# Performance work log

Hardware: AMD Instinct MI355X
Metric: run time of the kernel (lower is better)

The kernel has to match this reference:

```python
import jax, jax.numpy as jnp
import numpy as np

D_MODEL = 1024
D_FF = 1024
NUM_EXPERTS = 8
TOP_K = 2


def setup_inputs() -> dict:
    key = jax.random.key(0)
    ks = jax.random.split(key, 5)
    s_in = 1.0 / np.sqrt(D_MODEL)
    s_ff = 1.0 / np.sqrt(D_FF)
    return {
        "x": jax.random.normal(ks[0], (4, 2048, D_MODEL), dtype=jnp.float32),
        "gate_w": jax.random.normal(ks[1], (NUM_EXPERTS, D_MODEL), dtype=jnp.float32) * s_in,
        # torch Linear weight layout: [out_features, in_features], stacked over experts
        "w_gate": jax.random.normal(ks[2], (NUM_EXPERTS, D_FF, D_MODEL), dtype=jnp.float32) * s_in,
        "w_up": jax.random.normal(ks[3], (NUM_EXPERTS, D_FF, D_MODEL), dtype=jnp.float32) * s_in,
        "w_down": jax.random.normal(ks[4], (NUM_EXPERTS, D_MODEL, D_FF), dtype=jnp.float32) * s_ff,
    }


def reference(x, gate_w, w_gate, w_up, w_down):
    B, S, D = x.shape
    T = B * S
    E = gate_w.shape[0]
    xt = x.reshape(T, D)

    # Router
    logits = xt @ gate_w.T                      # [T, E]
    probs = jax.nn.softmax(logits, axis=-1)
    top_v, top_i = jax.lax.top_k(probs, TOP_K)  # [T, K]
    top_v = top_v / jnp.sum(top_v, axis=-1, keepdims=True)

    tokens_per_expert = jnp.sum(jax.nn.one_hot(top_i, E, dtype=jnp.float32), axis=(0, 1))  # [E]
    f = tokens_per_expert / jnp.sum(tokens_per_expert)
    P = jnp.mean(probs, axis=0)
    aux_loss = E * jnp.sum(f * P)

    # Combine weights: per-token weight for each expert (sum over top-k slots)
    combine = jnp.zeros((T, E), dtype=x.dtype).at[jnp.arange(T)[:, None], top_i].add(top_v)  # [T, E]

    # Dense per-expert SwiGLU (equivalent math to masked gather/scatter loop)
    g = jnp.einsum('td,efd->etf', xt, w_gate)   # [E, T, F]
    u = jnp.einsum('td,efd->etf', xt, w_up)     # [E, T, F]
    act = jax.nn.silu(g) * u
    eo = jnp.einsum('etf,edf->etd', act, w_down)  # [E, T, D]

    out = jnp.einsum('te,etd->td', combine, eo).reshape(B, S, D)
    return out, aux_loss, tokens_per_expert
```

## Files before the change

### kernel.cpp

```cpp
#include <hip/hip_runtime.h>


#define T_TOK   8192
#define DM      1024
#define DFF     1024
#define NE      8
#define TOTS    (2 * T_TOK)
#define R1_BLK  2048
#define CVT_BLK 2048

typedef __attribute__((ext_vector_type(8))) short bf16x8;
typedef __attribute__((ext_vector_type(4))) float f32x4;

#define ASYNC16(gp, lp) __builtin_amdgcn_global_load_lds( \
    (const __attribute__((address_space(1))) unsigned int*)(gp), \
    (__attribute__((address_space(3))) unsigned int*)(lp), 16, 0, 0)

__device__ __forceinline__ unsigned short f2bf(float f) {
    union { float f; unsigned u; } c; c.f = f;
    unsigned r = c.u + 0x7fffu + ((c.u >> 16) & 1u);
    return (unsigned short)(r >> 16);
}
__device__ __forceinline__ float bf2f(unsigned short h) {
    union { unsigned u; float f; } c; c.u = ((unsigned)h) << 16;
    return c.f;
}

__global__ __launch_bounds__(256) void pre_kernel(
    const float* __restrict__ x, const float* __restrict__ gate_w,
    const float* __restrict__ s0, const float* __restrict__ s1, const float* __restrict__ s2,
    unsigned short* __restrict__ d0, unsigned short* __restrict__ d1, unsigned short* __restrict__ d2,
    unsigned short* __restrict__ xb,
    int* __restrict__ topi, float2* __restrict__ topw, float* __restrict__ psum_part)
{
    int tid = threadIdx.x;
    int sub = blockIdx.x >> 1;

    if (blockIdx.x & 1) {
        int base = sub * 256 + tid;
        #pragma unroll
        for (int it = 0; it < 12; ++it) {
            int idx = base + it * (CVT_BLK * 256);
            int seg = idx >> 21;
            int off = (idx & ((1 << 21) - 1)) * 4;
            const float* s = (seg == 0) ? s0 : (seg == 1) ? s1 : s2;
            unsigned short* d = (seg == 0) ? d0 : (seg == 1) ? d1 : d2;
            float4 v = *(const float4*)(s + off);
            ushort4 o;
            o.x = f2bf(v.x); o.y = f2bf(v.y); o.z = f2bf(v.z); o.w = f2bf(v.w);
            *(ushort4*)(d + off) = o;
        }
        return;
    }

    __shared__ float gw[NE * DM];
    __shared__ float blk_psum[NE];

    for (int i = tid; i < NE * DM; i += 256) gw[i] = gate_w[i];
    if (tid < NE) blk_psum[tid] = 0.f;
    __syncthreads();

    int wv = tid >> 6, lane = tid & 63;
    int t = sub * 4 + wv;

    float acc[NE];
    #pragma unroll
    for (int e = 0; e < NE; ++e) acc[e] = 0.f;
    const float* xr = x + (size_t)t * DM;
    unsigned short* xbr = xb + (size_t)t * DM;
    #pragma unroll 4
    for (int i = 0; i < DM / 64; ++i) {
        float xv = xr[i * 64 + lane];
        xbr[i * 64 + lane] = f2bf(xv);
        #pragma unroll
        for (int e = 0; e < NE; ++e)
            acc[e] += xv * gw[e * DM + i * 64 + lane];
    }
    #pragma unroll
    for (int e = 0; e < NE; ++e) {
        float v = acc[e];
        #pragma unroll
        for (int s = 32; s > 0; s >>= 1) v += __shfl_xor(v, s, 64);
        acc[e] = v;
    }
    if (lane == 0) {
        float mx = acc[0];
        #pragma unroll
        for (int e = 1; e < NE; ++e) mx = fmaxf(mx, acc[e]);
        float p[NE], sum = 0.f;
        #pragma unroll
        for (int e = 0; e < NE; ++e) { p[e] = expf(acc[e] - mx); sum += p[e]; }
        float inv = 1.f / sum;
        #pragma unroll
        for (int e = 0; e < NE; ++e) { p[e] *= inv; atomicAdd(&blk_psum[e], p[e]); }
        int i1 = 0; float v1 = p[0];
        #pragma unroll
        for (int e = 1; e < NE; ++e) if (p[e] > v1) { v1 = p[e]; i1 = e; }
        int i2 = -1; float v2 = -1.f;
        #pragma unroll
        for (int e = 0; e < NE; ++e) { if (e == i1) continue; if (p[e] > v2) { v2 = p[e]; i2 = e; } }
        float winv = 1.f / (v1 + v2);
        topi[t] = i1 | (i2 << 8);
        topw[t] = make_float2(v1 * winv, v2 * winv);
    }
    __syncthreads();
    if (tid < NE) psum_part[sub * NE + tid] = blk_psum[tid];
}

__global__ __launch_bounds__(1024) void scatfin_kernel(
    const int* __restrict__ topi, const float* __restrict__ psum_part,
    int* __restrict__ elist, int2* __restrict__ cidx,
    int* __restrict__ ecnt, int* __restrict__ ebaseg, float* __restrict__ out_tail)
{
    __shared__ int lcnt[NE], run[NE], cb[NE], ebase[NE];
    __shared__ float parts[NE];
    __shared__ float red[1024];
    int tid = threadIdx.x;

    if (tid < NE) run[tid] = 0;
    __syncthreads();
    #pragma unroll
    for (int ch = 0; ch < T_TOK / 1024; ++ch) {
        int tt = ch * 1024 + tid;
        int pk = topi[tt];
        int e1 = pk & 0xff, e2 = (pk >> 8) & 0xff;
        if (tid < NE) lcnt[tid] = 0;
        __syncthreads();
        int p1 = atomicAdd(&lcnt[e1], 1);
        int p2 = atomicAdd(&lcnt[e2], 1);
        __syncthreads();
        if (tid < NE) { cb[tid] = run[tid]; run[tid] += lcnt[tid]; }
        __syncthreads();
        cidx[tt] = make_int2(cb[e1] + p1, cb[e2] + p2);
    }
    __syncthreads();
    if (tid == 0) {
        int s = 0;
        for (int e = 0; e < NE; ++e) { ebase[e] = s; s += run[e]; }
    }
    __syncthreads();
    #pragma unroll
    for (int ch = 0; ch < T_TOK / 1024; ++ch) {
        int tt = ch * 1024 + tid;
        int pk = topi[tt];
        int e1 = pk & 0xff, e2 = (pk >> 8) & 0xff;
        int2 pp = cidx[tt];
        int r1 = ebase[e1] + pp.x, r2 = ebase[e2] + pp.y;
        elist[r1] = tt;
        elist[r2] = tt;
        cidx[tt] = make_int2(r1, r2);
    }
    if (tid < NE) { ecnt[tid] = run[tid]; ebaseg[tid] = ebase[tid]; }

    int e = tid & 7, b0 = tid >> 3;
    float s = 0.f;
    for (int b = b0; b < R1_BLK; b += 128) s += psum_part[b * NE + e];
    red[tid] = s;
    __syncthreads();
    if (tid < NE) {
        float tot = 0.f;
        #pragma unroll
        for (int j = 0; j < 128; ++j) tot += red[tid + NE * j];
        float P = tot / (float)T_TOK;
        float f = (float)run[tid] / (float)(2 * T_TOK);
        parts[tid] = f * P;
        out_tail[1 + tid] = (float)run[tid];
    }
    __syncthreads();
    if (tid == 0) {
        float s2 = 0.f;
        for (int i = 0; i < NE; ++i) s2 += parts[i];
        out_tail[0] = (float)NE * s2;
    }
}

__global__ __launch_bounds__(256) void gemm1_kernel(
    const unsigned short* __restrict__ xb,
    const unsigned short* __restrict__ wgb,
    const unsigned short* __restrict__ wub,
    const int* __restrict__ elist, const int* __restrict__ ecnt,
    const int* __restrict__ ebaseg,
    unsigned short* __restrict__ Hbuf)
{
    int e = blockIdx.z, mt = blockIdx.y, ft = blockIdx.x;
    int ne = ecnt[e];
    if (mt * 128 >= ne) return;
    int base = ebaseg[e];

    __shared__ unsigned short As[128 * 64];
    __shared__ unsigned short Gs[64 * 64];
    __shared__ unsigned short Us[64 * 64];
    __shared__ int tok[128];

    int tid = threadIdx.x;
    if (tid < 128) {
        int slot = base + mt * 128 + tid;
        tok[tid] = elist[min(slot, TOTS - 1)];
    }
    __syncthreads();

    int wave = tid >> 6, lane = tid & 63;
    int quad = lane >> 4, col = lane & 15;
    int cr = tid >> 3;
    int cl = ((tid & 7) ^ (cr & 7)) * 8;

    const size_t woff = (size_t)e * (size_t)DFF * DM;
    const unsigned short* ap[4];
    #pragma unroll
    for (int j = 0; j < 4; ++j) ap[j] = xb + (size_t)tok[j * 32 + cr] * DM + cl;
    const unsigned short* gp[2];
    const unsigned short* up[2];
    #pragma unroll
    for (int j = 0; j < 2; ++j) {
        gp[j] = wgb + woff + (size_t)(ft * 64 + j * 32 + cr) * DM + cl;
        up[j] = wub + woff + (size_t)(ft * 64 + j * 32 + cr) * DM + cl;
    }
    unsigned short* lA = As + wave * 512;
    unsigned short* lG = Gs + wave * 512;
    unsigned short* lU = Us + wave * 512;

    f32x4 accG[2][4], accU[2][4];
    #pragma unroll
    for (int i = 0; i < 2; ++i)
        #pragma unroll
        for (int n = 0; n < 4; ++n) { accG[i][n] = (f32x4){0,0,0,0}; accU[i][n] = (f32x4){0,0,0,0}; }

    for (int k0 = 0; k0 < DM; k0 += 64) {
        __syncthreads();
        #pragma unroll
        for (int j = 0; j < 4; ++j) ASYNC16(ap[j] + k0, lA + j * 2048);
        #pragma unroll
        for (int j = 0; j < 2; ++j) {
            ASYNC16(gp[j] + k0, lG + j * 2048);
            ASYNC16(up[j] + k0, lU + j * 2048);
        }
        __syncthreads();
        #pragma unroll
        for (int ksoff = 0; ksoff < 8; ksoff += 4) {
            bf16x8 a[2], g[4], u[4];
            #pragma unroll
            for (int i = 0; i < 2; ++i) {
                int m = wave * 32 + i * 16 + col;
                a[i] = *(const bf16x8*)&As[m * 64 + ((quad + ksoff) ^ (m & 7)) * 8];
            }
            #pragma unroll
            for (int n = 0; n < 4; ++n) {
                int nb = n * 16 + col;
                int off = nb * 64 + ((quad + ksoff) ^ (nb & 7)) * 8;
                g[n] = *(const bf16x8*)&Gs[off];
                u[n] = *(const bf16x8*)&Us[off];
            }
            #pragma unroll
            for (int i = 0; i < 2; ++i)
                #pragma unroll
                for (int n = 0; n < 4; ++n) {
                    accG[i][n] = __builtin_amdgcn_mfma_f32_16x16x32_bf16(a[i], g[n], accG[i][n], 0, 0, 0);
                    accU[i][n] = __builtin_amdgcn_mfma_f32_16x16x32_bf16(a[i], u[n], accU[i][n], 0, 0, 0);
                }
        }
    }
    #pragma unroll
    for (int i = 0; i < 2; ++i) {
        #pragma unroll
        for (int r = 0; r < 4; ++r) {
            int pos = mt * 128 + wave * 32 + i * 16 + quad * 4 + r;
            if (pos >= ne) continue;
            unsigned short* hr = Hbuf + (size_t)(base + pos) * DFF + ft * 64 + col;
            #pragma unroll
            for (int n = 0; n < 4; ++n) {
                float gg = accG[i][n][r], uu = accU[i][n][r];
                float h = (gg / (1.f + expf(-gg))) * uu;
                hr[n * 16] = f2bf(h);
            }
        }
    }
}

__global__ __launch_bounds__(256) void gemm2_kernel(
    const unsigned short* __restrict__ Hbuf,
    const unsigned short* __restrict__ wdb,
    const int* __restrict__ ecnt, const int* __restrict__ ebaseg,
    unsigned short* __restrict__ eo)
{
    int e = blockIdx.z, mt = blockIdx.y, dt = blockIdx.x;
    int ne = ecnt[e];
    if (mt * 128 >= ne) return;
    int base = ebaseg[e];

    __shared__ unsigned short As[128 * 64];
    __shared__ unsigned short Bs[128 * 64];

    int tid = threadIdx.x;
    int wave = tid >> 6, lane = tid & 63;
    int quad = lane >> 4, col = lane & 15;
    int wr = (wave >> 1) * 64, wc = (wave & 1) * 64;
    int cr = tid >> 3;
    int cl = ((tid & 7) ^ (cr & 7)) * 8;

    const size_t woff = (size_t)e * (size_t)DM * DFF;
    const unsigned short* ap[4];
    const unsigned short* bp[4];
    #pragma unroll
    for (int j = 0; j < 4; ++j) {
        int hrow = min(base + mt * 128 + j * 32 + cr, TOTS - 1);
        ap[j] = Hbuf + (size_t)hrow * DFF + cl;
        bp[j] = wdb + woff + (size_t)(dt * 128 + j * 32 + cr) * DFF + cl;
    }
    unsigned short* lA = As + wave * 512;
    unsigned short* lB = Bs + wave * 512;

    f32x4 acc[4][4];
    #pragma unroll
    for (int i = 0; i < 4; ++i)
        #pragma unroll
        for (int n = 0; n < 4; ++n) acc[i][n] = (f32x4){0,0,0,0};

    for (int k0 = 0; k0 < DFF; k0 += 64) {
        __syncthreads();
        #pragma unroll
        for (int j = 0; j < 4; ++j) {
            ASYNC16(ap[j] + k0, lA + j * 2048);
            ASYNC16(bp[j] + k0, lB + j * 2048);
        }
        __syncthreads();
        #pragma unroll
        for (int ksoff = 0; ksoff < 8; ksoff += 4) {
            bf16x8 a[4], b[4];
            #pragma unroll
            for (int i = 0; i < 4; ++i) {
                int m = wr + i * 16 + col;
                a[i] = *(const bf16x8*)&As[m * 64 + ((quad + ksoff) ^ (m & 7)) * 8];
            }
            #pragma unroll
            for (int n = 0; n < 4; ++n) {
                int nb = wc + n * 16 + col;
                b[n] = *(const bf16x8*)&Bs[nb * 64 + ((quad + ksoff) ^ (nb & 7)) * 8];
            }
            #pragma unroll
            for (int i = 0; i < 4; ++i)
                #pragma unroll
                for (int n = 0; n < 4; ++n)
                    acc[i][n] = __builtin_amdgcn_mfma_f32_16x16x32_bf16(a[i], b[n], acc[i][n], 0, 0, 0);
        }
    }
    #pragma unroll
    for (int i = 0; i < 4; ++i) {
        #pragma unroll
        for (int r = 0; r < 4; ++r) {
            int pos = mt * 128 + wr + i * 16 + quad * 4 + r;
            if (pos >= ne) continue;
            unsigned short* er = eo + (size_t)(base + pos) * DM + dt * 128 + wc + col;
            #pragma unroll
            for (int n = 0; n < 4; ++n)
                er[n * 16] = f2bf(acc[i][n][r]);
        }
    }
}

__global__ __launch_bounds__(256) void combine_kernel(
    const unsigned short* __restrict__ eo, const float2* __restrict__ topw,
    const int2* __restrict__ cidx, float* __restrict__ out)
{
    int idx = blockIdx.x * 256 + threadIdx.x;
    int t = idx >> 7;
    int c = (idx & 127) << 3;
    float2 w = topw[t];
    int2 rr = cidx[t];
    const unsigned short* p0 = eo + (size_t)rr.x * DM + c;
    const unsigned short* p1 = eo + (size_t)rr.y * DM + c;
    ushort4 a0 = *(const ushort4*)p0;
    ushort4 a1 = *(const ushort4*)(p0 + 4);
    ushort4 b0 = *(const ushort4*)p1;
    ushort4 b1 = *(const ushort4*)(p1 + 4);
    float* orow = out + (size_t)t * DM + c;
    float4 o0, o1;
    o0.x = w.x * bf2f(a0.x) + w.y * bf2f(b0.x);
    o0.y = w.x * bf2f(a0.y) + w.y * bf2f(b0.y);
    o0.z = w.x * bf2f(a0.z) + w.y * bf2f(b0.z);
    o0.w = w.x * bf2f(a0.w) + w.y * bf2f(b0.w);
    o1.x = w.x * bf2f(a1.x) + w.y * bf2f(b1.x);
    o1.y = w.x * bf2f(a1.y) + w.y * bf2f(b1.y);
    o1.z = w.x * bf2f(a1.z) + w.y * bf2f(b1.z);
    o1.w = w.x * bf2f(a1.w) + w.y * bf2f(b1.w);
    *(float4*)orow = o0;
    *(float4*)(orow + 4) = o1;
}

extern "C" void kernel_launch(void* const* d_in, const int* in_sizes, int n_in,
                              void* d_out, int out_size, void* d_ws, size_t ws_size,
                              hipStream_t stream) {
    const float* x      = (const float*)d_in[0];
    const float* gate_w = (const float*)d_in[1];
    const float* w_gate = (const float*)d_in[2];
    const float* w_up   = (const float*)d_in[3];
    const float* w_down = (const float*)d_in[4];
    float* out = (float*)d_out;

    char* p = (char*)d_ws;
    unsigned short* xb   = (unsigned short*)p; p += (size_t)T_TOK * DM * 2;
    unsigned short* wgb  = (unsigned short*)p; p += (size_t)NE * DFF * DM * 2;
    unsigned short* wub  = (unsigned short*)p; p += (size_t)NE * DFF * DM * 2;
    unsigned short* wdb  = (unsigned short*)p; p += (size_t)NE * DM * DFF * 2;
    unsigned short* Hbuf = (unsigned short*)p; p += (size_t)TOTS * DFF * 2;
    int*   elist = (int*)p;   p += (size_t)TOTS * 4;
    int*   ecnt  = (int*)p;   p += NE * 4;
    int*   ebaseg= (int*)p;   p += NE * 4;
    int*   topi  = (int*)p;   p += (size_t)T_TOK * 4;
    float2* topw = (float2*)p; p += (size_t)T_TOK * 8;
    int2*  cidx  = (int2*)p;  p += (size_t)T_TOK * 8;
    float* psum_part = (float*)p; p += (size_t)R1_BLK * NE * 4;
    unsigned short* eo = wgb;

    pre_kernel<<<R1_BLK + CVT_BLK, 256, 0, stream>>>(
        x, gate_w, w_gate, w_up, w_down, wgb, wub, wdb,
        xb, topi, topw, psum_part);
    scatfin_kernel<<<1, 1024, 0, stream>>>(topi, psum_part, elist, cidx, ecnt, ebaseg,
                                           out + (size_t)T_TOK * DM);
    gemm1_kernel<<<dim3(DFF / 64, TOTS / 128, NE), 256, 0, stream>>>(
        xb, wgb, wub, elist, ecnt, ebaseg, Hbuf);
    gemm2_kernel<<<dim3(DM / 128, TOTS / 128, NE), 256, 0, stream>>>(
        Hbuf, wdb, ecnt, ebaseg, eo);
    combine_kernel<<<T_TOK * DM / 8 / 256, 256, 0, stream>>>(eo, topw, cidx, out);
}
```

Baseline: 340.0 us.

## Double-buffer LDS tiles in both expert GEMM kernels to overlap loads with MFMA

Both grouped GEMM kernels now keep two LDS buffers per operand and use a ping-pong main loop. The async global-to-LDS copy of the next K-slice is issued before the MFMA work on the current slice, so load latency can hide behind compute instead of stalling at each barrier. In exchange, LDS use per block doubles (to 64KB in gemm2), which may lower the number of resident blocks per CU. The loop is hardcoded to 16 K-steps of 64.

```diff
diff --git a/kernel.cpp b/kernel.cpp
--- a/kernel.cpp
+++ b/kernel.cpp
@@ -174,6 +174,42 @@
     }
 }
 
+#define G1_STAGE(BUF, KS) do { \
+    _Pragma("unroll") \
+    for (int j = 0; j < 4; ++j) ASYNC16(ap[j] + (KS), &As[BUF][wave * 512] + j * 2048); \
+    _Pragma("unroll") \
+    for (int j = 0; j < 2; ++j) { \
+        ASYNC16(gp[j] + (KS), &Gs[BUF][wave * 512] + j * 2048); \
+        ASYNC16(up[j] + (KS), &Us[BUF][wave * 512] + j * 2048); \
+    } \
+} while (0)
+
+#define G1_COMP(BUF) do { \
+    _Pragma("unroll") \
+    for (int ksoff = 0; ksoff < 8; ksoff += 4) { \
+        bf16x8 a[2], g[4], u[4]; \
+        _Pragma("unroll") \
+        for (int i = 0; i < 2; ++i) { \
+            int m = wave * 32 + i * 16 + col; \
+            a[i] = *(const bf16x8*)&As[BUF][m * 64 + ((quad + ksoff) ^ (m & 7)) * 8]; \
+        } \
+        _Pragma("unroll") \
+        for (int n = 0; n < 4; ++n) { \
+            int nb = n * 16 + col; \
+            int off = nb * 64 + ((quad + ksoff) ^ (nb & 7)) * 8; \
+            g[n] = *(const bf16x8*)&Gs[BUF][off]; \
+            u[n] = *(const bf16x8*)&Us[BUF][off]; \
+        } \
+        _Pragma("unroll") \
+        for (int i = 0; i < 2; ++i) \
+            _Pragma("unroll") \
+            for (int n = 0; n < 4; ++n) { \
+                accG[i][n] = __builtin_amdgcn_mfma_f32_16x16x32_bf16(a[i], g[n], accG[i][n], 0, 0, 0); \
+                accU[i][n] = __builtin_amdgcn_mfma_f32_16x16x32_bf16(a[i], u[n], accU[i][n], 0, 0, 0); \
+            } \
+    } \
+} while (0)
+
 __global__ __launch_bounds__(256) void gemm1_kernel(
     const unsigned short* __restrict__ xb,
     const unsigned short* __restrict__ wgb,
@@ -187,9 +223,9 @@
     if (mt * 128 >= ne) return;
     int base = ebaseg[e];
 
-    __shared__ unsigned short As[128 * 64];
-    __shared__ unsigned short Gs[64 * 64];
-    __shared__ unsigned short Us[64 * 64];
+    __shared__ unsigned short As[2][128 * 64];
+    __shared__ unsigned short Gs[2][64 * 64];
+    __shared__ unsigned short Us[2][64 * 64];
     __shared__ int tok[128];
 
     int tid = threadIdx.x;
@@ -215,9 +251,6 @@
         gp[j] = wgb + woff + (size_t)(ft * 64 + j * 32 + cr) * DM + cl;
         up[j] = wub + woff + (size_t)(ft * 64 + j * 32 + cr) * DM + cl;
     }
-    unsigned short* lA = As + wave * 512;
-    unsigned short* lG = Gs + wave * 512;
-    unsigned short* lU = Us + wave * 512;
 
     f32x4 accG[2][4], accU[2][4];
     #pragma unroll
@@ -225,40 +258,16 @@
         #pragma unroll
         for (int n = 0; n < 4; ++n) { accG[i][n] = (f32x4){0,0,0,0}; accU[i][n] = (f32x4){0,0,0,0}; }
 
-    for (int k0 = 0; k0 < DM; k0 += 64) {
-        __syncthreads();
-        #pragma unroll
-        for (int j = 0; j < 4; ++j) ASYNC16(ap[j] + k0, lA + j * 2048);
-        #pragma unroll
-        for (int j = 0; j < 2; ++j) {
-            ASYNC16(gp[j] + k0, lG + j * 2048);
-            ASYNC16(up[j] + k0, lU + j * 2048);
-        }
-        __syncthreads();
-        #pragma unroll
-        for (int ksoff = 0; ksoff < 8; ksoff += 4) {
-            bf16x8 a[2], g[4], u[4];
-            #pragma unroll
-            for (int i = 0; i < 2; ++i) {
-                int m = wave * 32 + i * 16 + col;
-                a[i] = *(const bf16x8*)&As[m * 64 + ((quad + ksoff) ^ (m & 7)) * 8];
-            }
-            #pragma unroll
-            for (int n = 0; n < 4; ++n) {
-                int nb = n * 16 + col;
-                int off = nb * 64 + ((quad + ksoff) ^ (nb & 7)) * 8;
-                g[n] = *(const bf16x8*)&Gs[off];
-                u[n] = *(const bf16x8*)&Us[off];
-            }
-            #pragma unroll
-            for (int i = 0; i < 2; ++i)
-                #pragma unroll
-                for (int n = 0; n < 4; ++n) {
-                    accG[i][n] = __builtin_amdgcn_mfma_f32_16x16x32_bf16(a[i], g[n], accG[i][n], 0, 0, 0);
-                    accU[i][n] = __builtin_amdgcn_mfma_f32_16x16x32_bf16(a[i], u[n], accU[i][n], 0, 0, 0);
-                }
-        }
-    }
+    G1_STAGE(0, 0);
+    for (int tt = 0; tt < 8; ++tt) {
+        __syncthreads();
+        G1_STAGE(1, (2 * tt + 1) * 64);
+        G1_COMP(0);
+        __syncthreads();
+        if (tt < 7) G1_STAGE(0, (2 * tt + 2) * 64);
+        G1_COMP(1);
+    }
+
     #pragma unroll
     for (int i = 0; i < 2; ++i) {
         #pragma unroll
@@ -276,6 +285,36 @@
     }
 }
 
+#define G2_STAGE(BUF, KS) do { \
+    _Pragma("unroll") \
+    for (int j = 0; j < 4; ++j) { \
+        ASYNC16(ap[j] + (KS), &As[BUF][wave * 512] + j * 2048); \
+        ASYNC16(bp[j] + (KS), &Bs[BUF][wave * 512] + j * 2048); \
+    } \
+} while (0)
+
+#define G2_COMP(BUF) do { \
+    _Pragma("unroll") \
+    for (int ksoff = 0; ksoff < 8; ksoff += 4) { \
+        bf16x8 a[4], b[4]; \
+        _Pragma("unroll") \
+        for (int i = 0; i < 4; ++i) { \
+            int m = wr + i * 16 + col; \
+            a[i] = *(const bf16x8*)&As[BUF][m * 64 + ((quad + ksoff) ^ (m & 7)) * 8]; \
+        } \
+        _Pragma("unroll") \
+        for (int n = 0; n < 4; ++n) { \
+            int nb = wc + n * 16 + col; \
+            b[n] = *(const bf16x8*)&Bs[BUF][nb * 64 + ((quad + ksoff) ^ (nb & 7)) * 8]; \
+        } \
+        _Pragma("unroll") \
+        for (int i = 0; i < 4; ++i) \
+            _Pragma("unroll") \
+            for (int n = 0; n < 4; ++n) \
+                acc[i][n] = __builtin_amdgcn_mfma_f32_16x16x32_bf16(a[i], b[n], acc[i][n], 0, 0, 0); \
+    } \
+} while (0)
+
 __global__ __launch_bounds__(256) void gemm2_kernel(
     const unsigned short* __restrict__ Hbuf,
     const unsigned short* __restrict__ wdb,
@@ -287,8 +326,8 @@
     if (mt * 128 >= ne) return;
     int base = ebaseg[e];
 
-    __shared__ unsigned short As[128 * 64];
-    __shared__ unsigned short Bs[128 * 64];
+    __shared__ unsigned short As[2][128 * 64];
+    __shared__ unsigned short Bs[2][128 * 64];
 
     int tid = threadIdx.x;
     int wave = tid >> 6, lane = tid & 63;
@@ -306,8 +345,6 @@
         ap[j] = Hbuf + (size_t)hrow * DFF + cl;
         bp[j] = wdb + woff + (size_t)(dt * 128 + j * 32 + cr) * DFF + cl;
     }
-    unsigned short* lA = As + wave * 512;
-    unsigned short* lB = Bs + wave * 512;
 
     f32x4 acc[4][4];
     #pragma unroll
@@ -315,34 +352,16 @@
         #pragma unroll
         for (int n = 0; n < 4; ++n) acc[i][n] = (f32x4){0,0,0,0};
 
-    for (int k0 = 0; k0 < DFF; k0 += 64) {
-        __syncthreads();
-        #pragma unroll
-        for (int j = 0; j < 4; ++j) {
-            ASYNC16(ap[j] + k0, lA + j * 2048);
-            ASYNC16(bp[j] + k0, lB + j * 2048);
-        }
-        __syncthreads();
-        #pragma unroll
-        for (int ksoff = 0; ksoff < 8; ksoff += 4) {
-            bf16x8 a[4], b[4];
-            #pragma unroll
-            for (int i = 0; i < 4; ++i) {
-                int m = wr + i * 16 + col;
-                a[i] = *(const bf16x8*)&As[m * 64 + ((quad + ksoff) ^ (m & 7)) * 8];
-            }
-            #pragma unroll
-            for (int n = 0; n < 4; ++n) {
-                int nb = wc + n * 16 + col;
-                b[n] = *(const bf16x8*)&Bs[nb * 64 + ((quad + ksoff) ^ (nb & 7)) * 8];
-            }
-            #pragma unroll
-            for (int i = 0; i < 4; ++i)
-                #pragma unroll
-                for (int n = 0; n < 4; ++n)
-                    acc[i][n] = __builtin_amdgcn_mfma_f32_16x16x32_bf16(a[i], b[n], acc[i][n], 0, 0, 0);
-        }
-    }
+    G2_STAGE(0, 0);
+    for (int tt = 0; tt < 8; ++tt) {
+        __syncthreads();
+        G2_STAGE(1, (2 * tt + 1) * 64);
+        G2_COMP(0);
+        __syncthreads();
+        if (tt < 7) G2_STAGE(0, (2 * tt + 2) * 64);
+        G2_COMP(1);
+    }
+
     #pragma unroll
     for (int i = 0; i < 4; ++i) {
         #pragma unroll
```

Result: slower. 363.9 us (+7.0%).

## Parallelize routing scatter across experts and retile gemm1 waves as 2x2

Applied to the files above, without the earlier changes.

The single-block scatter kernel with per-chunk atomics and many barriers is replaced by one block per expert. Each block builds per-thread expert histograms, reduces and prefix-scans them, then writes that expert's slots in token order, and block 0 computes the aux loss. Separately, gemm1 waves are rearranged from a 4x1 to a 2x2 layout (64 rows by 32 columns each), so each wave loads 4 A fragments and 2 G/U fragments instead of 2 and 4. This cuts LDS reads per MFMA and shortens the serial routing stage, at the cost of every block rereading topi.

```diff
diff --git a/kernel.cpp b/kernel.cpp
--- a/kernel.cpp
+++ b/kernel.cpp
@@ -107,70 +107,105 @@
     if (tid < NE) psum_part[sub * NE + tid] = blk_psum[tid];
 }
 
-__global__ __launch_bounds__(1024) void scatfin_kernel(
+__global__ __launch_bounds__(256) void scatfin_kernel(
     const int* __restrict__ topi, const float* __restrict__ psum_part,
     int* __restrict__ elist, int2* __restrict__ cidx,
     int* __restrict__ ecnt, int* __restrict__ ebaseg, float* __restrict__ out_tail)
 {
-    __shared__ int lcnt[NE], run[NE], cb[NE], ebase[NE];
-    __shared__ float parts[NE];
-    __shared__ float red[1024];
+    __shared__ int c8[256 * NE];
+    __shared__ int sm[256];
+    __shared__ int ebase_sh[NE + 1];
+    __shared__ float f8[256 * NE];
+
+    int e = blockIdx.x;
     int tid = threadIdx.x;
 
-    if (tid < NE) run[tid] = 0;
+    int cnt8[NE];
+    #pragma unroll
+    for (int j = 0; j < NE; ++j) cnt8[j] = 0;
+    #pragma unroll 4
+    for (int k = 0; k < 32; ++k) {
+        int pk = topi[tid * 32 + k];
+        cnt8[pk & 0xff]++;
+        cnt8[(pk >> 8) & 0xff]++;
+    }
+    #pragma unroll
+    for (int j = 0; j < NE; ++j) c8[tid * NE + j] = cnt8[j];
+    sm[tid] = cnt8[e];
     __syncthreads();
-    #pragma unroll
-    for (int ch = 0; ch < T_TOK / 1024; ++ch) {
-        int tt = ch * 1024 + tid;
+
+    for (int s = 128; s > 0; s >>= 1) {
+        if (tid < s) {
+            #pragma unroll
+            for (int j = 0; j < NE; ++j)
+                c8[tid * NE + j] += c8[(tid + s) * NE + j];
+        }
+        __syncthreads();
+    }
+    if (tid == 0) {
+        int s = 0;
+        for (int j = 0; j < NE; ++j) { ebase_sh[j] = s; s += c8[j]; }
+        ebase_sh[NE] = s;
+    }
+    int mymatch = cnt8[e];
+    __syncthreads();
+    for (int s = 1; s < 256; s <<= 1) {
+        int v = (tid >= s) ? sm[tid - s] : 0;
+        __syncthreads();
+        sm[tid] += v;
+        __syncthreads();
+    }
+    int wbase = ebase_sh[e] + sm[tid] - mymatch;
+
+    for (int k = 0; k < 32; ++k) {
+        int tt = tid * 32 + k;
         int pk = topi[tt];
         int e1 = pk & 0xff, e2 = (pk >> 8) & 0xff;
-        if (tid < NE) lcnt[tid] = 0;
-        __syncthreads();
-        int p1 = atomicAdd(&lcnt[e1], 1);
-        int p2 = atomicAdd(&lcnt[e2], 1);
-        __syncthreads();
-        if (tid < NE) { cb[tid] = run[tid]; run[tid] += lcnt[tid]; }
-        __syncthreads();
-        cidx[tt] = make_int2(cb[e1] + p1, cb[e2] + p2);
-    }
-    __syncthreads();
+        if (e1 == e) {
+            elist[wbase] = tt;
+            ((int*)cidx)[2 * tt] = wbase;
+            wbase++;
+        } else if (e2 == e) {
+            elist[wbase] = tt;
+            ((int*)cidx)[2 * tt + 1] = wbase;
+            wbase++;
+        }
+    }
     if (tid == 0) {
-        int s = 0;
-        for (int e = 0; e < NE; ++e) { ebase[e] = s; s += run[e]; }
-    }
-    __syncthreads();
-    #pragma unroll
-    for (int ch = 0; ch < T_TOK / 1024; ++ch) {
-        int tt = ch * 1024 + tid;
-        int pk = topi[tt];
-        int e1 = pk & 0xff, e2 = (pk >> 8) & 0xff;
-        int2 pp = cidx[tt];
-        int r1 = ebase[e1] + pp.x, r2 = ebase[e2] + pp.y;
-        elist[r1] = tt;
-        elist[r2] = tt;
-        cidx[tt] = make_int2(r1, r2);
-    }
-    if (tid < NE) { ecnt[tid] = run[tid]; ebaseg[tid] = ebase[tid]; }
-
-    int e = tid & 7, b0 = tid >> 3;
-    float s = 0.f;
-    for (int b = b0; b < R1_BLK; b += 128) s += psum_part[b * NE + e];
-    red[tid] = s;
-    __syncthreads();
-    if (tid < NE) {
-        float tot = 0.f;
-        #pragma unroll
-        for (int j = 0; j < 128; ++j) tot += red[tid + NE * j];
-        float P = tot / (float)T_TOK;
-        float f = (float)run[tid] / (float)(2 * T_TOK);
-        parts[tid] = f * P;
-        out_tail[1 + tid] = (float)run[tid];
-    }
-    __syncthreads();
-    if (tid == 0) {
-        float s2 = 0.f;
-        for (int i = 0; i < NE; ++i) s2 += parts[i];
-        out_tail[0] = (float)NE * s2;
+        ecnt[e]   = c8[e];
+        ebaseg[e] = ebase_sh[e];
+    }
+
+    if (e == 0) {
+        float s8[NE];
+        #pragma unroll
+        for (int j = 0; j < NE; ++j) s8[j] = 0.f;
+        for (int b = tid; b < R1_BLK; b += 256) {
+            const float* row = psum_part + (size_t)b * NE;
+            #pragma unroll
+            for (int j = 0; j < NE; ++j) s8[j] += row[j];
+        }
+        #pragma unroll
+        for (int j = 0; j < NE; ++j) f8[tid * NE + j] = s8[j];
+        __syncthreads();
+        for (int s = 128; s > 0; s >>= 1) {
+            if (tid < s) {
+                #pragma unroll
+                for (int j = 0; j < NE; ++j)
+                    f8[tid * NE + j] += f8[(tid + s) * NE + j];
+            }
+            __syncthreads();
+        }
+        if (tid == 0) {
+            float aux = 0.f;
+            for (int j = 0; j < NE; ++j) {
+                float P = f8[j] / (float)T_TOK;
+                float f = (float)c8[j] / (float)(2 * T_TOK);
+                aux += f * P;
+                out_tail[1 + j] = (float)c8[j];
+            }
+            out_tail[0] = (float)NE * aux;
+        }
     }
 }
 
@@ -200,6 +235,7 @@
     __syncthreads();
 
     int wave = tid >> 6, lane = tid & 63;
+    int wm = wave >> 1, wn = wave & 1;
     int quad = lane >> 4, col = lane & 15;
     int cr = tid >> 3;
     int cl = ((tid & 7) ^ (cr & 7)) * 8;
@@ -219,11 +255,11 @@
     unsigned short* lG = Gs + wave * 512;
     unsigned short* lU = Us + wave * 512;
 
-    f32x4 accG[2][4], accU[2][4];
-    #pragma unroll
-    for (int i = 0; i < 2; ++i)
-        #pragma unroll
-        for (int n = 0; n < 4; ++n) { accG[i][n] = (f32x4){0,0,0,0}; accU[i][n] = (f32x4){0,0,0,0}; }
+    f32x4 accG[4][2], accU[4][2];
+    #pragma unroll
+    for (int i = 0; i < 4; ++i)
+        #pragma unroll
+        for (int n = 0; n < 2; ++n) { accG[i][n] = (f32x4){0,0,0,0}; accU[i][n] = (f32x4){0,0,0,0}; }
 
     for (int k0 = 0; k0 < DM; k0 += 64) {
         __syncthreads();
@@ -237,37 +273,37 @@
         __syncthreads();
         #pragma unroll
         for (int ksoff = 0; ksoff < 8; ksoff += 4) {
-            bf16x8 a[2], g[4], u[4];
-            #pragma unroll
-            for (int i = 0; i < 2; ++i) {
-                int m = wave * 32 + i * 16 + col;
+            bf16x8 a[4], g[2], u[2];
+            #pragma unroll
+            for (int i = 0; i < 4; ++i) {
+                int m = wm * 64 + i * 16 + col;
                 a[i] = *(const bf16x8*)&As[m * 64 + ((quad + ksoff) ^ (m & 7)) * 8];
             }
             #pragma unroll
-            for (int n = 0; n < 4; ++n) {
-                int nb = n * 16 + col;
+            for (int n = 0; n < 2; ++n) {
+                int nb = wn * 32 + n * 16 + col;
                 int off = nb * 64 + ((quad + ksoff) ^ (nb & 7)) * 8;
                 g[n] = *(const bf16x8*)&Gs[off];
                 u[n] = *(const bf16x8*)&Us[off];
             }
             #pragma unroll
-            for (int i = 0; i < 2; ++i)
+            for (int i = 0; i < 4; ++i)
                 #pragma unroll
-                for (int n = 0; n < 4; ++n) {
+                for (int n = 0; n < 2; ++n) {
                     accG[i][n] = __builtin_amdgcn_mfma_f32_16x16x32_bf16(a[i], g[n], accG[i][n], 0, 0, 0);
                     accU[i][n] = __builtin_amdgcn_mfma_f32_16x16x32_bf16(a[i], u[n], accU[i][n], 0, 0, 0);
                 }
         }
     }
     #pragma unroll
-    for (int i = 0; i < 2; ++i) {
+    for (int i = 0; i < 4; ++i) {
         #pragma unroll
         for (int r = 0; r < 4; ++r) {
-            int pos = mt * 128 + wave * 32 + i * 16 + quad * 4 + r;
+            int pos = mt * 128 + wm * 64 + i * 16 + quad * 4 + r;
             if (pos >= ne) continue;
-            unsigned short* hr = Hbuf + (size_t)(base + pos) * DFF + ft * 64 + col;
-            #pragma unroll
-            for (int n = 0; n < 4; ++n) {
+            unsigned short* hr = Hbuf + (size_t)(base + pos) * DFF + ft * 64 + wn * 32 + col;
+            #pragma unroll
+            for (int n = 0; n < 2; ++n) {
                 float gg = accG[i][n][r], uu = accU[i][n][r];
                 float h = (gg / (1.f + expf(-gg))) * uu;
                 hr[n * 16] = f2bf(h);
@@ -414,7 +450,7 @@
     pre_kernel<<<R1_BLK + CVT_BLK, 256, 0, stream>>>(
         x, gate_w, w_gate, w_up, w_down, wgb, wub, wdb,
         xb, topi, topw, psum_part);
-    scatfin_kernel<<<1, 1024, 0, stream>>>(topi, psum_part, elist, cidx, ecnt, ebaseg,
+    scatfin_kernel<<<NE, 256, 0, stream>>>(topi, psum_part, elist, cidx, ecnt, ebaseg,
                                            out + (size_t)T_TOK * DM);
     gemm1_kernel<<<dim3(DFF / 64, TOTS / 128, NE), 256, 0, stream>>>(
         xb, wgb, wub, elist, ecnt, ebaseg, Hbuf);
```

After: 362.1 us. 1.06x slower.
